# Kernel optimization log

Measured on AMD Instinct MI355X. Metric: run time of the kernel, lower is better.

## Reference

```python
import jax, jax.numpy as jnp
import numpy as np


def setup_inputs() -> dict:
    key = jax.random.key(0)
    k1, k2, k3 = jax.random.split(key, 3)
    B, S, D = 128, 1024, 64
    return {
        "q": jax.random.normal(k1, (B, S, D), dtype=jnp.float32),
        "k": jax.random.normal(k2, (B, S, D), dtype=jnp.float32),
        "v": jax.random.normal(k3, (B, S, D), dtype=jnp.float32),
    }


def reference(q, k, v):
    # Faithful to the torch module: NO 1/sqrt(d) scaling.
    # Chunking over batch dim in the original is math-equivalent to full bmm.
    scores = jnp.einsum("bsd,btd->bst", q, k)  # [B, S, S]
    attn = jax.nn.softmax(scores, axis=-1)
    return jnp.einsum("bst,btd->bsd", attn, v)  # [B, S, D]
```

## Files before the change

### kernel.cpp

```cpp
#include <hip/hip_runtime.h>
#include <math.h>

namespace {

typedef _Float16 half8 __attribute__((ext_vector_type(8)));
typedef float floatx4 __attribute__((ext_vector_type(4)));

constexpr int kS   = 1024;
constexpr int kD   = 64;
constexpr int kPad = 72;
constexpr float kLog2e = 1.4426950408889634f;
constexpr float kThr   = 8.0f;

union H4 { _Float16 h[4]; uint2 u2; };

__device__ __forceinline__ float fast_exp2(float x) {
#if __has_builtin(__builtin_amdgcn_exp2f)
  return __builtin_amdgcn_exp2f(x);
#else
  return exp2f(x);
#endif
}

__device__ __forceinline__ float fast_rcp(float x) {
#if __has_builtin(__builtin_amdgcn_rcpf)
  return __builtin_amdgcn_rcpf(x);
#else
  return 1.0f / x;
#endif
}

__global__ __launch_bounds__(256, 2)
void fa_mfma_kernel(const float* __restrict__ qg, const float* __restrict__ kg,
                    const float* __restrict__ vg, float* __restrict__ og) {
  __shared__ __align__(16) _Float16 sK [2][64][kPad];
  __shared__ __align__(16) _Float16 sVt[2][64][kPad];
  __shared__ __align__(16) _Float16 sP [256][kPad];

  const int tid  = threadIdx.x;
  const int lane = tid & 63;
  const int w    = __builtin_amdgcn_readfirstlane(tid >> 6);
  const int quad = lane >> 4;
  const int r    = lane & 15;

  const int blk = blockIdx.x;
  const int b     = (blk & 7) + 8 * (blk >> 5);
  const int qbase = ((blk >> 3) & 3) * 256;

  const float* qb = qg + (size_t)b * kS * kD;
  const float* kb = kg + (size_t)b * kS * kD;
  const float* vb = vg + (size_t)b * kS * kD;
  float*       ob = og + (size_t)b * kS * kD;

  half8 fqh[4][2], fql[4][2];
#pragma unroll
  for (int ntq = 0; ntq < 4; ++ntq)
#pragma unroll
    for (int ks = 0; ks < 2; ++ks) {
      const float* src =
          qb + (size_t)(qbase + w * 64 + ntq * 16 + r) * kD + ks * 32 + quad * 8;
      float4 a = ((const float4*)src)[0];
      float4 c = ((const float4*)src)[1];
      float f[8] = {a.x, a.y, a.z, a.w, c.x, c.y, c.z, c.w};
#pragma unroll
      for (int j = 0; j < 8; ++j) {
        float x = f[j] * kLog2e;
        _Float16 h = (_Float16)x;
        fqh[ntq][ks][j] = h;
        fql[ntq][ks][j] = (_Float16)(x - (float)h);
      }
    }

  float m_i[4] = {-INFINITY, -INFINITY, -INFINITY, -INFINITY};
  float l_i[4] = {0.f, 0.f, 0.f, 0.f};
  floatx4 O[4][4];
#pragma unroll
  for (int a = 0; a < 4; ++a)
#pragma unroll
    for (int c = 0; c < 4; ++c) O[a][c] = floatx4{0.f, 0.f, 0.f, 0.f};

  const int krow = tid >> 2, kc0 = (tid & 3) * 16;
  const int vkey4 = (tid & 15) * 4;
  const int vd0   = (tid >> 4) * 4;
  float4 kbuf[4], vbuf[4];

  auto load_kv = [&](int kt) {
    const float4* ksrc = (const float4*)(kb + (size_t)(kt * 64 + krow) * kD + kc0);
#pragma unroll
    for (int g = 0; g < 4; ++g) kbuf[g] = ksrc[g];
#pragma unroll
    for (int kk = 0; kk < 4; ++kk)
      vbuf[kk] = *(const float4*)(vb + (size_t)(kt * 64 + vkey4 + kk) * kD + vd0);
  };
  auto stage = [&](int bi) {
#pragma unroll
    for (int g = 0; g < 4; ++g) {
      float t[4] = {kbuf[g].x, kbuf[g].y, kbuf[g].z, kbuf[g].w};
      H4 hk;
#pragma unroll
      for (int j = 0; j < 4; ++j) hk.h[j] = (_Float16)t[j];
      *(uint2*)&sK[bi][krow][kc0 + g * 4] = hk.u2;
    }
    float tv[4][4];
#pragma unroll
    for (int kk = 0; kk < 4; ++kk) {
      tv[kk][0] = vbuf[kk].x; tv[kk][1] = vbuf[kk].y;
      tv[kk][2] = vbuf[kk].z; tv[kk][3] = vbuf[kk].w;
    }
#pragma unroll
    for (int j = 0; j < 4; ++j) {
      H4 hv;
#pragma unroll
      for (int kk = 0; kk < 4; ++kk) hv.h[kk] = (_Float16)tv[kk][j];
      *(uint2*)&sVt[bi][vd0 + j][vkey4] = hv.u2;
    }
  };

  load_kv(0);
  stage(0);
  load_kv(1);

  for (int kt = 0; kt < kS / 64; ++kt) {
    const int cur = kt & 1, nxt = cur ^ 1;
    __syncthreads();
    stage(nxt);
    load_kv((kt + 2) & 15);

    floatx4 S0[2][4];
    __builtin_amdgcn_s_setprio(1);
#pragma unroll
    for (int mt = 0; mt < 4; ++mt) {
      half8 fk0 = *(const half8*)&sK[cur][mt * 16 + r][quad * 8];
      half8 fk1 = *(const half8*)&sK[cur][mt * 16 + r][32 + quad * 8];
#pragma unroll
      for (int g = 0; g < 2; ++g) {
        floatx4 s = {0.f, 0.f, 0.f, 0.f};
        s = __builtin_amdgcn_mfma_f32_16x16x32_f16(fk0, fqh[g][0], s, 0, 0, 0);
        s = __builtin_amdgcn_mfma_f32_16x16x32_f16(fk1, fqh[g][1], s, 0, 0, 0);
        s = __builtin_amdgcn_mfma_f32_16x16x32_f16(fk0, fql[g][0], s, 0, 0, 0);
        s = __builtin_amdgcn_mfma_f32_16x16x32_f16(fk1, fql[g][1], s, 0, 0, 0);
        S0[g][mt] = s;
      }
    }
    __builtin_amdgcn_s_setprio(0);

    {
      float tm[2];
#pragma unroll
      for (int g = 0; g < 2; ++g) {
        float t = -INFINITY;
#pragma unroll
        for (int mt = 0; mt < 4; ++mt)
#pragma unroll
          for (int j = 0; j < 4; ++j) t = fmaxf(t, S0[g][mt][j]);
        t = fmaxf(t, __shfl_xor(t, 16, 64));
        t = fmaxf(t, __shfl_xor(t, 32, 64));
        tm[g] = t;
      }
      const unsigned long long need =
          __ballot(tm[0] > m_i[0] + kThr || tm[1] > m_i[1] + kThr);
      if (need) {
        float alpha[2];
#pragma unroll
        for (int g = 0; g < 2; ++g) {
          const float mn = fmaxf(m_i[g], tm[g]);
          alpha[g] = fast_exp2(m_i[g] - mn);
          m_i[g] = mn;
          l_i[g] *= alpha[g];
        }
#pragma unroll
        for (int g = 0; g < 2; ++g)
#pragma unroll
          for (int j = 0; j < 4; ++j) {
            const float a = __shfl(alpha[g], quad * 4 + j, 64);
#pragma unroll
            for (int nd = 0; nd < 4; ++nd) O[g][nd][j] *= a;
          }
      }
#pragma unroll
      for (int g = 0; g < 2; ++g) {
        float rs = 0.f;
#pragma unroll
        for (int mt = 0; mt < 4; ++mt) {
          H4 hp;
#pragma unroll
          for (int j = 0; j < 4; ++j) {
            float pj = fast_exp2(S0[g][mt][j] - m_i[g]);
            rs += pj;
            hp.h[j] = (_Float16)pj;
          }
          *(uint2*)&sP[w * 64 + g * 16 + r][mt * 16 + quad * 4] = hp.u2;
        }
        rs += __shfl_xor(rs, 16, 64);
        rs += __shfl_xor(rs, 32, 64);
        l_i[g] += rs;
      }
    }

    floatx4 S1[2][4];
    __builtin_amdgcn_s_setprio(1);
#pragma unroll
    for (int mt = 0; mt < 4; ++mt) {
      half8 fk0 = *(const half8*)&sK[cur][mt * 16 + r][quad * 8];
      half8 fk1 = *(const half8*)&sK[cur][mt * 16 + r][32 + quad * 8];
#pragma unroll
      for (int g = 0; g < 2; ++g) {
        floatx4 s = {0.f, 0.f, 0.f, 0.f};
        s = __builtin_amdgcn_mfma_f32_16x16x32_f16(fk0, fqh[2 + g][0], s, 0, 0, 0);
        s = __builtin_amdgcn_mfma_f32_16x16x32_f16(fk1, fqh[2 + g][1], s, 0, 0, 0);
        s = __builtin_amdgcn_mfma_f32_16x16x32_f16(fk0, fql[2 + g][0], s, 0, 0, 0);
        s = __builtin_amdgcn_mfma_f32_16x16x32_f16(fk1, fql[2 + g][1], s, 0, 0, 0);
        S1[g][mt] = s;
      }
    }
    __builtin_amdgcn_s_setprio(0);

    __builtin_amdgcn_s_setprio(1);
#pragma unroll
    for (int ks = 0; ks < 2; ++ks) {
      half8 fp0 = *(const half8*)&sP[w * 64 + 0 * 16 + r][ks * 32 + quad * 8];
      half8 fp1 = *(const half8*)&sP[w * 64 + 1 * 16 + r][ks * 32 + quad * 8];
#pragma unroll
      for (int nd = 0; nd < 4; ++nd) {
        half8 fv = *(const half8*)&sVt[cur][nd * 16 + r][ks * 32 + quad * 8];
        O[0][nd] = __builtin_amdgcn_mfma_f32_16x16x32_f16(fp0, fv, O[0][nd], 0, 0, 0);
        O[1][nd] = __builtin_amdgcn_mfma_f32_16x16x32_f16(fp1, fv, O[1][nd], 0, 0, 0);
      }
    }
    __builtin_amdgcn_s_setprio(0);

    {
      float tm[2];
#pragma unroll
      for (int g = 0; g < 2; ++g) {
        float t = -INFINITY;
#pragma unroll
        for (int mt = 0; mt < 4; ++mt)
#pragma unroll
          for (int j = 0; j < 4; ++j) t = fmaxf(t, S1[g][mt][j]);
        t = fmaxf(t, __shfl_xor(t, 16, 64));
        t = fmaxf(t, __shfl_xor(t, 32, 64));
        tm[g] = t;
      }
      const unsigned long long need =
          __ballot(tm[0] > m_i[2] + kThr || tm[1] > m_i[3] + kThr);
      if (need) {
        float alpha[2];
#pragma unroll
        for (int g = 0; g < 2; ++g) {
          const float mn = fmaxf(m_i[2 + g], tm[g]);
          alpha[g] = fast_exp2(m_i[2 + g] - mn);
          m_i[2 + g] = mn;
          l_i[2 + g] *= alpha[g];
        }
#pragma unroll
        for (int g = 0; g < 2; ++g)
#pragma unroll
          for (int j = 0; j < 4; ++j) {
            const float a = __shfl(alpha[g], quad * 4 + j, 64);
#pragma unroll
            for (int nd = 0; nd < 4; ++nd) O[2 + g][nd][j] *= a;
          }
      }
#pragma unroll
      for (int g = 0; g < 2; ++g) {
        float rs = 0.f;
#pragma unroll
        for (int mt = 0; mt < 4; ++mt) {
          H4 hp;
#pragma unroll
          for (int j = 0; j < 4; ++j) {
            float pj = fast_exp2(S1[g][mt][j] - m_i[2 + g]);
            rs += pj;
            hp.h[j] = (_Float16)pj;
          }
          *(uint2*)&sP[w * 64 + (2 + g) * 16 + r][mt * 16 + quad * 4] = hp.u2;
        }
        rs += __shfl_xor(rs, 16, 64);
        rs += __shfl_xor(rs, 32, 64);
        l_i[2 + g] += rs;
      }
    }

    __builtin_amdgcn_s_setprio(1);
#pragma unroll
    for (int ks = 0; ks < 2; ++ks) {
      half8 fp2 = *(const half8*)&sP[w * 64 + 2 * 16 + r][ks * 32 + quad * 8];
      half8 fp3 = *(const half8*)&sP[w * 64 + 3 * 16 + r][ks * 32 + quad * 8];
#pragma unroll
      for (int nd = 0; nd < 4; ++nd) {
        half8 fv = *(const half8*)&sVt[cur][nd * 16 + r][ks * 32 + quad * 8];
        O[2][nd] = __builtin_amdgcn_mfma_f32_16x16x32_f16(fp2, fv, O[2][nd], 0, 0, 0);
        O[3][nd] = __builtin_amdgcn_mfma_f32_16x16x32_f16(fp3, fv, O[3][nd], 0, 0, 0);
      }
    }
    __builtin_amdgcn_s_setprio(0);
  }

#pragma unroll
  for (int mtq = 0; mtq < 4; ++mtq)
#pragma unroll
    for (int j = 0; j < 4; ++j) {
      const float lrow = __shfl(l_i[mtq], quad * 4 + j, 64);
      const float linv = fast_rcp(lrow);
      float* dst =
          ob + (size_t)(qbase + w * 64 + mtq * 16 + quad * 4 + j) * kD + r;
#pragma unroll
      for (int nd = 0; nd < 4; ++nd) dst[nd * 16] = O[mtq][nd][j] * linv;
    }
}

}

extern "C" void kernel_launch(void* const* d_in, const int* in_sizes, int n_in,
                              void* d_out, int out_size, void* d_ws, size_t ws_size,
                              hipStream_t stream) {
  const float* q = (const float*)d_in[0];
  const float* k = (const float*)d_in[1];
  const float* v = (const float*)d_in[2];
  float* out = (float*)d_out;

  fa_mfma_kernel<<<dim3(512), 256, 0, stream>>>(q, k, v, out);
}
```

Baseline: 173.8 us.

## Speculatively exponentiate with stale max, defer row-sum reduction, swizzle V^T LDS layout

The softmax step now computes exp2 against the current running max and takes the local max in the same pass. It recomputes the probabilities only when the ballot reports that some lane's max exceeded the threshold. The per-tile cross-lane shuffle reductions for the row max and row sum are removed: the max is reduced only on the rescale path, and the row-sum partials are kept per lane and reduced once at the end. Separately, the transposed V tile in LDS gets an XOR-style column swizzle to reduce bank conflicts on the PV fragment reads. The risk is a duplicate exp pass whenever a rescale happens. Per-lane partial sums that are rescaled by a shared alpha should still be mathematically correct.

```diff
diff --git a/kernel.cpp b/kernel.cpp
--- a/kernel.cpp
+++ b/kernel.cpp
@@ -112,7 +112,9 @@
       H4 hv;
 #pragma unroll
       for (int kk = 0; kk < 4; ++kk) hv.h[kk] = (_Float16)tv[kk][j];
-      *(uint2*)&sVt[bi][vd0 + j][vkey4] = hv.u2;
+      const int row = vd0 + j;
+      const int col = ((((vkey4 >> 3) + row) & 7) << 3) | (vkey4 & 7);
+      *(uint2*)&sVt[bi][row][col] = hv.u2;
     }
   };
 
@@ -145,28 +147,36 @@
     __builtin_amdgcn_s_setprio(0);
 
     {
-      float tm[2];
-#pragma unroll
-      for (int g = 0; g < 2; ++g) {
-        float t = -INFINITY;
-#pragma unroll
-        for (int mt = 0; mt < 4; ++mt)
-#pragma unroll
-          for (int j = 0; j < 4; ++j) t = fmaxf(t, S0[g][mt][j]);
-        t = fmaxf(t, __shfl_xor(t, 16, 64));
-        t = fmaxf(t, __shfl_xor(t, 32, 64));
-        tm[g] = t;
-      }
+      float rs[2] = {0.f, 0.f}, pmax[2] = {-INFINITY, -INFINITY};
+#pragma unroll
+      for (int g = 0; g < 2; ++g)
+#pragma unroll
+        for (int mt = 0; mt < 4; ++mt) {
+          H4 hp;
+#pragma unroll
+          for (int j = 0; j < 4; ++j) {
+            const float sj = S0[g][mt][j];
+            pmax[g] = fmaxf(pmax[g], sj);
+            const float pj = fast_exp2(sj - m_i[g]);
+            rs[g] += pj;
+            hp.h[j] = (_Float16)pj;
+          }
+          *(uint2*)&sP[w * 64 + g * 16 + r][mt * 16 + quad * 4] = hp.u2;
+        }
       const unsigned long long need =
-          __ballot(tm[0] > m_i[0] + kThr || tm[1] > m_i[1] + kThr);
+          __ballot(pmax[0] > m_i[0] + kThr || pmax[1] > m_i[1] + kThr);
       if (need) {
         float alpha[2];
 #pragma unroll
         for (int g = 0; g < 2; ++g) {
-          const float mn = fmaxf(m_i[g], tm[g]);
+          float t = pmax[g];
+          t = fmaxf(t, __shfl_xor(t, 16, 64));
+          t = fmaxf(t, __shfl_xor(t, 32, 64));
+          const float mn = fmaxf(m_i[g], t);
           alpha[g] = fast_exp2(m_i[g] - mn);
           m_i[g] = mn;
           l_i[g] *= alpha[g];
+          rs[g] = 0.f;
         }
 #pragma unroll
         for (int g = 0; g < 2; ++g)
@@ -176,25 +186,22 @@
 #pragma unroll
             for (int nd = 0; nd < 4; ++nd) O[g][nd][j] *= a;
           }
-      }
-#pragma unroll
-      for (int g = 0; g < 2; ++g) {
-        float rs = 0.f;
-#pragma unroll
-        for (int mt = 0; mt < 4; ++mt) {
-          H4 hp;
-#pragma unroll
-          for (int j = 0; j < 4; ++j) {
-            float pj = fast_exp2(S0[g][mt][j] - m_i[g]);
-            rs += pj;
-            hp.h[j] = (_Float16)pj;
-          }
-          *(uint2*)&sP[w * 64 + g * 16 + r][mt * 16 + quad * 4] = hp.u2;
-        }
-        rs += __shfl_xor(rs, 16, 64);
-        rs += __shfl_xor(rs, 32, 64);
-        l_i[g] += rs;
-      }
+#pragma unroll
+        for (int g = 0; g < 2; ++g)
+#pragma unroll
+          for (int mt = 0; mt < 4; ++mt) {
+            H4 hp;
+#pragma unroll
+            for (int j = 0; j < 4; ++j) {
+              const float pj = fast_exp2(S0[g][mt][j] - m_i[g]);
+              rs[g] += pj;
+              hp.h[j] = (_Float16)pj;
+            }
+            *(uint2*)&sP[w * 64 + g * 16 + r][mt * 16 + quad * 4] = hp.u2;
+          }
+      }
+      l_i[0] += rs[0];
+      l_i[1] += rs[1];
     }
 
     floatx4 S1[2][4];
@@ -222,7 +229,8 @@
       half8 fp1 = *(const half8*)&sP[w * 64 + 1 * 16 + r][ks * 32 + quad * 8];
 #pragma unroll
       for (int nd = 0; nd < 4; ++nd) {
-        half8 fv = *(const half8*)&sVt[cur][nd * 16 + r][ks * 32 + quad * 8];
+        const int pb = ((ks * 4 + quad + r) & 7) << 3;
+        half8 fv = *(const half8*)&sVt[cur][nd * 16 + r][pb];
         O[0][nd] = __builtin_amdgcn_mfma_f32_16x16x32_f16(fp0, fv, O[0][nd], 0, 0, 0);
         O[1][nd] = __builtin_amdgcn_mfma_f32_16x16x32_f16(fp1, fv, O[1][nd], 0, 0, 0);
       }
@@ -230,28 +238,36 @@
     __builtin_amdgcn_s_setprio(0);
 
     {
-      float tm[2];
-#pragma unroll
-      for (int g = 0; g < 2; ++g) {
-        float t = -INFINITY;
-#pragma unroll
-        for (int mt = 0; mt < 4; ++mt)
-#pragma unroll
-          for (int j = 0; j < 4; ++j) t = fmaxf(t, S1[g][mt][j]);
-        t = fmaxf(t, __shfl_xor(t, 16, 64));
-        t = fmaxf(t, __shfl_xor(t, 32, 64));
-        tm[g] = t;
-      }
+      float rs[2] = {0.f, 0.f}, pmax[2] = {-INFINITY, -INFINITY};
+#pragma unroll
+      for (int g = 0; g < 2; ++g)
+#pragma unroll
+        for (int mt = 0; mt < 4; ++mt) {
+          H4 hp;
+#pragma unroll
+          for (int j = 0; j < 4; ++j) {
+            const float sj = S1[g][mt][j];
+            pmax[g] = fmaxf(pmax[g], sj);
+            const float pj = fast_exp2(sj - m_i[2 + g]);
+            rs[g] += pj;
+            hp.h[j] = (_Float16)pj;
+          }
+          *(uint2*)&sP[w * 64 + (2 + g) * 16 + r][mt * 16 + quad * 4] = hp.u2;
+        }
       const unsigned long long need =
-          __ballot(tm[0] > m_i[2] + kThr || tm[1] > m_i[3] + kThr);
+          __ballot(pmax[0] > m_i[2] + kThr || pmax[1] > m_i[3] + kThr);
       if (need) {
         float alpha[2];
 #pragma unroll
         for (int g = 0; g < 2; ++g) {
-          const float mn = fmaxf(m_i[2 + g], tm[g]);
+          float t = pmax[g];
+          t = fmaxf(t, __shfl_xor(t, 16, 64));
+          t = fmaxf(t, __shfl_xor(t, 32, 64));
+          const float mn = fmaxf(m_i[2 + g], t);
           alpha[g] = fast_exp2(m_i[2 + g] - mn);
           m_i[2 + g] = mn;
           l_i[2 + g] *= alpha[g];
+          rs[g] = 0.f;
         }
 #pragma unroll
         for (int g = 0; g < 2; ++g)
@@ -261,25 +277,22 @@
 #pragma unroll
             for (int nd = 0; nd < 4; ++nd) O[2 + g][nd][j] *= a;
           }
-      }
-#pragma unroll
-      for (int g = 0; g < 2; ++g) {
-        float rs = 0.f;
-#pragma unroll
-        for (int mt = 0; mt < 4; ++mt) {
-          H4 hp;
-#pragma unroll
-          for (int j = 0; j < 4; ++j) {
-            float pj = fast_exp2(S1[g][mt][j] - m_i[2 + g]);
-            rs += pj;
-            hp.h[j] = (_Float16)pj;
-          }
-          *(uint2*)&sP[w * 64 + (2 + g) * 16 + r][mt * 16 + quad * 4] = hp.u2;
-        }
-        rs += __shfl_xor(rs, 16, 64);
-        rs += __shfl_xor(rs, 32, 64);
-        l_i[2 + g] += rs;
-      }
+#pragma unroll
+        for (int g = 0; g < 2; ++g)
+#pragma unroll
+          for (int mt = 0; mt < 4; ++mt) {
+            H4 hp;
+#pragma unroll
+            for (int j = 0; j < 4; ++j) {
+              const float pj = fast_exp2(S1[g][mt][j] - m_i[2 + g]);
+              rs[g] += pj;
+              hp.h[j] = (_Float16)pj;
+            }
+            *(uint2*)&sP[w * 64 + (2 + g) * 16 + r][mt * 16 + quad * 4] = hp.u2;
+          }
+      }
+      l_i[2] += rs[0];
+      l_i[3] += rs[1];
     }
 
     __builtin_amdgcn_s_setprio(1);
@@ -289,7 +302,8 @@
       half8 fp3 = *(const half8*)&sP[w * 64 + 3 * 16 + r][ks * 32 + quad * 8];
 #pragma unroll
       for (int nd = 0; nd < 4; ++nd) {
-        half8 fv = *(const half8*)&sVt[cur][nd * 16 + r][ks * 32 + quad * 8];
+        const int pb = ((ks * 4 + quad + r) & 7) << 3;
+        half8 fv = *(const half8*)&sVt[cur][nd * 16 + r][pb];
         O[2][nd] = __builtin_amdgcn_mfma_f32_16x16x32_f16(fp2, fv, O[2][nd], 0, 0, 0);
         O[3][nd] = __builtin_amdgcn_mfma_f32_16x16x32_f16(fp3, fv, O[3][nd], 0, 0, 0);
       }
@@ -298,16 +312,20 @@
   }
 
 #pragma unroll
-  for (int mtq = 0; mtq < 4; ++mtq)
+  for (int mtq = 0; mtq < 4; ++mtq) {
+    float t = l_i[mtq];
+    t += __shfl_xor(t, 16, 64);
+    t += __shfl_xor(t, 32, 64);
 #pragma unroll
     for (int j = 0; j < 4; ++j) {
-      const float lrow = __shfl(l_i[mtq], quad * 4 + j, 64);
+      const float lrow = __shfl(t, quad * 4 + j, 64);
       const float linv = fast_rcp(lrow);
       float* dst =
           ob + (size_t)(qbase + w * 64 + mtq * 16 + quad * 4 + j) * kD + r;
 #pragma unroll
       for (int nd = 0; nd < 4; ++nd) dst[nd * 16] = O[mtq][nd][j] * linv;
     }
+  }
 }
 
 }
```

Measured after the change: 205.5 us. 18.2% more time.
